# Performance work log

Hardware: AMD Instinct MI355X
Metric: run time of the kernel (lower is better)

The kernel has to match this reference:

```python
import jax, jax.numpy as jnp
import numpy as np

HIDDEN = 2048
HEADS = 16
KV_LORA = 512
ROPE_D = 64
NOPE_D = ROPE_D          # module sets qk_nope_head_dim = qk_rope_head_dim
Q_HEAD_D = ROPE_D + NOPE_D
V_D = 128
B, S = 2, 2048
SCALE = ROPE_D ** -0.5


def setup_inputs() -> dict:
    key = jax.random.key(0)
    ks = jax.random.split(key, 6)
    hidden_state = jax.random.normal(ks[0], (B, S, HIDDEN), dtype=jnp.float32)
    attention_mask = jnp.zeros((1, 1, S, S), dtype=jnp.float32)
    s = 0.02
    W_down = jax.random.normal(ks[1], (HIDDEN, KV_LORA + ROPE_D), dtype=jnp.float32) * s
    W_up = jax.random.normal(ks[2], (KV_LORA, HEADS * (NOPE_D + V_D)), dtype=jnp.float32) * s
    W_q = jax.random.normal(ks[3], (HIDDEN, HEADS * Q_HEAD_D), dtype=jnp.float32) * s
    W_o = jax.random.normal(ks[4], (HEADS * V_D, HIDDEN), dtype=jnp.float32) * s
    return {"hidden_state": hidden_state, "attention_mask": attention_mask,
            "W_down": W_down, "W_up": W_up, "W_q": W_q, "W_o": W_o}


def reference(hidden_state, attention_mask, W_down, W_up, W_q, W_o):
    b, s, _ = hidden_state.shape
    # low-rank KV down-projection; split latent and shared rope key
    kv_down = hidden_state @ W_down                      # [b,s,kv_lora+rope]
    kv_compressed = kv_down[..., :KV_LORA]
    k_rope = kv_down[..., KV_LORA:]                      # [b,s,rope]
    # up-project latent to per-head nope-key and value
    kv = (kv_compressed @ W_up).reshape(b, s, HEADS, NOPE_D + V_D)
    kv = kv.transpose(0, 2, 1, 3)                        # [b,h,s,nope+v]
    k_nope = kv[..., :NOPE_D]
    v = kv[..., NOPE_D:]
    # queries
    q = (hidden_state @ W_q).reshape(b, s, HEADS, Q_HEAD_D).transpose(0, 2, 1, 3)
    q_rope = q[..., :ROPE_D]
    q_nope = q[..., ROPE_D:]
    q_full = jnp.concatenate([q_rope, q_nope], axis=-1)  # [b,h,s,2d]
    # broadcast shared rope key across heads and concat with per-head nope key
    k_rope_exp = jnp.broadcast_to(k_rope[:, None], (b, HEADS, s, ROPE_D))
    k_full = jnp.concatenate([k_rope_exp, k_nope], axis=-1)
    scores = jnp.einsum('bhqd,bhkd->bhqk', q_full, k_full) * SCALE
    scores = scores + attention_mask
    probs = jax.nn.softmax(scores, axis=-1)
    ctx = jnp.einsum('bhqk,bhkd->bhqd', probs, v)        # [b,h,s,v]
    ctx = ctx.transpose(0, 2, 1, 3).reshape(b, s, HEADS * V_D)
    return ctx @ W_o
```

## Files before the change

kernel.cpp:

```cpp
#include <hip/hip_runtime.h>
#include <hip/hip_bf16.h>

#define HEADS   16
#define S_LEN   2048
#define BATCH   2
#define MTOT    (BATCH * S_LEN)
#define HIDDEN  2048
#define SCALE   0.125f
#define QKD_LD  2688

typedef __attribute__((ext_vector_type(8))) short          bf16x8;
typedef __attribute__((ext_vector_type(8))) unsigned short u16x8;
typedef __attribute__((ext_vector_type(4))) unsigned short u16x4;
typedef __attribute__((ext_vector_type(4))) float          f32x4;

__device__ __forceinline__ unsigned short f2bf(float f) {
    union { float f; unsigned u; } v; v.f = f;
    unsigned r = v.u + 0x7FFFu + ((v.u >> 16) & 1u);
    return (unsigned short)(r >> 16);
}

__device__ __forceinline__ unsigned cvtpk(float a, float b) {
    unsigned r;
    asm("v_cvt_pk_bf16_f32 %0, %1, %2" : "=v"(r) : "v"(a), "v"(b));
    return r;
}

__device__ __forceinline__ void gld16(const void* g, const void* l) {
    __builtin_amdgcn_global_load_lds(
        (const __attribute__((address_space(1))) void*)g,
        (__attribute__((address_space(3))) void*)l, 16, 0, 0);
}

__global__ __launch_bounds__(256)
void cast_bf16(const float* __restrict__ in, unsigned short* __restrict__ out)
{
    const size_t i = ((size_t)blockIdx.x * 256 + threadIdx.x) * 8;
    float4 a = *(const float4*)&in[i];
    float4 b = *(const float4*)&in[i + 4];
    u16x8 o;
    o[0] = f2bf(a.x); o[1] = f2bf(a.y); o[2] = f2bf(a.z); o[3] = f2bf(a.w);
    o[4] = f2bf(b.x); o[5] = f2bf(b.y); o[6] = f2bf(b.z); o[7] = f2bf(b.w);
    *(u16x8*)&out[i] = o;
}

__global__ __launch_bounds__(256)
void tc_w(const float* __restrict__ W, int N, int K, unsigned short* __restrict__ Wt)
{
    __shared__ float Tf[64][68];
    const int t  = threadIdx.x;
    const int n0 = blockIdx.x * 64, k0 = blockIdx.y * 64;
    if (n0 >= N) {
        u16x8 z = {0,0,0,0,0,0,0,0};
#pragma unroll
        for (int ii = 0; ii < 2; ii++) {
            int idx = t + 256 * ii;
            int rn = idx >> 3, c8 = (idx & 7) * 8;
            *(u16x8*)&Wt[(size_t)(n0 + rn) * K + k0 + c8] = z;
        }
        return;
    }
#pragma unroll
    for (int ii = 0; ii < 4; ii++) {
        int idx = t + 256 * ii;
        int rk = idx >> 4, c4 = (idx & 15) * 4;
        *(float4*)&Tf[rk][c4] = *(const float4*)&W[(size_t)(k0 + rk) * N + n0 + c4];
    }
    __syncthreads();
#pragma unroll
    for (int ii = 0; ii < 2; ii++) {
        int idx = t + 256 * ii;
        int rn = idx >> 3, c8 = (idx & 7) * 8;
        u16x8 o;
#pragma unroll
        for (int j = 0; j < 8; j++) o[j] = f2bf(Tf[c8 + j][rn]);
        *(u16x8*)&Wt[(size_t)(n0 + rn) * K + k0 + c8] = o;
    }
}

__global__ __launch_bounds__(256)
void transpose_v(const unsigned short* __restrict__ kvu, unsigned short* __restrict__ vT)
{
    __shared__ unsigned short Ts[64][80];
    const int t  = threadIdx.x;
    const int s0 = blockIdx.x * 64;
    const int h  = blockIdx.y >> 1, d0 = (blockIdx.y & 1) * 64;
    const int b  = blockIdx.z;
    const size_t base = (size_t)b * S_LEN;
#pragma unroll
    for (int ii = 0; ii < 2; ii++) {
        int idx = t + 256 * ii;
        int rs = idx >> 3, c8 = (idx & 7) * 8;
        *(u16x8*)&Ts[rs][c8] =
            *(const u16x8*)&kvu[(base + s0 + rs) * 3072 + h * 192 + 64 + d0 + c8];
    }
    __syncthreads();
    const size_t bh = (size_t)(b * HEADS + h);
#pragma unroll
    for (int ii = 0; ii < 2; ii++) {
        int idx = t + 256 * ii;
        int rd = idx >> 3, c8 = (idx & 7) * 8;
        u16x8 o;
#pragma unroll
        for (int j = 0; j < 8; j++) o[j] = Ts[c8 + j][rd];
        *(u16x8*)&vT[(bh * 128 + d0 + rd) * S_LEN + s0 + c8] = o;
    }
}

template<bool OUT_BF16>
__global__ __launch_bounds__(256)
void gemm_bf16(const unsigned short* __restrict__ A, int lda, int K,
               const unsigned short* __restrict__ Bt,
               void* __restrict__ C, int N, int ldc)
{
    __shared__ unsigned short As[128 * 32];
    __shared__ unsigned short Bs[128 * 32];
    const int t = threadIdx.x, lane = t & 63, w = t >> 6;
    const int l15 = lane & 15, lg = lane >> 4;
    const int row0 = blockIdx.y * 128, col0 = blockIdx.x * 128;
    const int wr = w >> 1, wc = w & 1;

    f32x4 acc[4][4] = {};

    for (int k0 = 0; k0 < K; k0 += 32) {
        __syncthreads();
#pragma unroll
        for (int ii = 0; ii < 2; ii++) {
            int u = (ii * 4 + w) * 64 + lane;
            gld16(&A[(size_t)(row0 + (u >> 2)) * lda + k0 + (u & 3) * 8],
                  (char*)As + (ii * 4 + w) * 1024);
            gld16(&Bt[(size_t)(col0 + (u >> 2)) * K + k0 + (u & 3) * 8],
                  (char*)Bs + (ii * 4 + w) * 1024);
        }
        __syncthreads();
        bf16x8 af[4], bb[4];
#pragma unroll
        for (int m = 0; m < 4; m++)
            af[m] = *(const bf16x8*)&As[(wr * 64 + m * 16 + l15) * 32 + lg * 8];
#pragma unroll
        for (int n = 0; n < 4; n++)
            bb[n] = *(const bf16x8*)&Bs[(wc * 64 + n * 16 + l15) * 32 + lg * 8];
#pragma unroll
        for (int m = 0; m < 4; m++)
#pragma unroll
            for (int n = 0; n < 4; n++)
                acc[m][n] = __builtin_amdgcn_mfma_f32_16x16x32_bf16(
                    af[m], bb[n], acc[m][n], 0, 0, 0);
    }

#pragma unroll
    for (int m = 0; m < 4; m++)
#pragma unroll
        for (int n = 0; n < 4; n++) {
            int col = col0 + wc * 64 + n * 16 + l15;
            if (col < N) {
#pragma unroll
                for (int r = 0; r < 4; r++) {
                    int row = row0 + wr * 64 + m * 16 + lg * 4 + r;
                    if (OUT_BF16)
                        ((unsigned short*)C)[(size_t)row * ldc + col] = f2bf(acc[m][n][r]);
                    else
                        ((float*)C)[(size_t)row * ldc + col] = acc[m][n][r];
                }
            }
        }
}

__global__ __launch_bounds__(256, 2)
void mla_attn_mfma(const unsigned short* __restrict__ qkd,
                   const unsigned short* __restrict__ kvu,
                   const unsigned short* __restrict__ vT,
                   const float* __restrict__ mask,
                   unsigned short* __restrict__ ctxb)
{
    __shared__ unsigned short KV[2][64 * 128 + 128 * 64];
    __shared__ unsigned short Pl[4][32 * 64];
    const int t = threadIdx.x, lane = t & 63, w = t >> 6;
    const int l15 = lane & 15, lg = lane >> 4;
    const int h = blockIdx.y, b = blockIdx.z;
    const int q0 = blockIdx.x * 128 + w * 32;
    const size_t base = (size_t)b * S_LEN;
    const size_t bh = (size_t)(b * HEADS + h);
    const unsigned short* qb = qkd + 640;
    unsigned short* Pw = &Pl[w][0];
    const unsigned psw = (unsigned)(l15 & 7) << 4;

    bf16x8 qf[2][4];
#pragma unroll
    for (int m = 0; m < 2; m++)
#pragma unroll
        for (int kk = 0; kk < 4; kk++)
            qf[m][kk] = *(const bf16x8*)&qb[(base + q0 + m * 16 + l15) * QKD_LD
                                            + h * 128 + kk * 32 + lg * 8];

    f32x4 octx[2][8] = {};
    float mrun[2] = {-INFINITY, -INFINITY};
    float lrun[2] = {0.f, 0.f};

    const float* mrow0 = &mask[(size_t)(q0 + l15) * S_LEN + lg * 4];
    const float* mrow1 = mrow0 + (size_t)16 * S_LEN;

    auto STAGE = [&](int buf, int s0) {
        unsigned short* Kb = &KV[buf][0];
        unsigned short* Vb = &KV[buf][64 * 128];
#pragma unroll
        for (int ii = 0; ii < 4; ii++) {
            int u = (ii * 4 + w) * 64 + lane;
            {
                int row = u >> 4, x = u & 15, y = x ^ (row & 7);
                const unsigned short* g = (y < 8)
                    ? &qkd[(base + s0 + row) * QKD_LD + 512 + y * 8]
                    : &kvu[(base + s0 + row) * 3072 + h * 192 + (y - 8) * 8];
                gld16(g, (char*)Kb + (ii * 4 + w) * 1024);
            }
            {
                int d = u >> 3, x = u & 7, y = x ^ (d & 7);
                gld16(&vT[(bh * 128 + d) * S_LEN + s0 + y * 8],
                      (char*)Vb + (ii * 4 + w) * 1024);
            }
        }
    };

    const int NT = S_LEN / 64;
    STAGE(0, 0);

    for (int kt = 0; kt < NT; kt++) {
        const int cur = kt & 1;
        const int s0 = kt * 64;
        const unsigned short* Ks = &KV[cur][0];
        const unsigned short* Vs = &KV[cur][64 * 128];

        __builtin_amdgcn_s_barrier();

        float4 mv[2][4];
#pragma unroll
        for (int n = 0; n < 4; n++) {
            mv[0][n] = *(const float4*)&mrow0[s0 + n * 16];
            mv[1][n] = *(const float4*)&mrow1[s0 + n * 16];
        }
        __builtin_amdgcn_sched_barrier(0);

        if (kt + 1 < NT) {
            STAGE(cur ^ 1, s0 + 64);
            __builtin_amdgcn_sched_barrier(0);
            asm volatile("s_waitcnt vmcnt(16)" ::: "memory");
        } else {
            __builtin_amdgcn_sched_barrier(0);
            asm volatile("s_waitcnt vmcnt(8)" ::: "memory");
        }
        __builtin_amdgcn_sched_barrier(0);
        __builtin_amdgcn_s_barrier();

        f32x4 sc[2][4] = {};
        __builtin_amdgcn_s_setprio(1);
#pragma unroll
        for (int n = 0; n < 4; n++) {
            const int key = n * 16 + l15;
#pragma unroll
            for (int kk = 0; kk < 4; kk++) {
                const int x = (kk * 4 + lg) ^ (key & 7);
                bf16x8 kf = *(const bf16x8*)&Ks[key * 128 + x * 8];
                sc[0][n] = __builtin_amdgcn_mfma_f32_16x16x32_bf16(kf, qf[0][kk], sc[0][n], 0, 0, 0);
                sc[1][n] = __builtin_amdgcn_mfma_f32_16x16x32_bf16(kf, qf[1][kk], sc[1][n], 0, 0, 0);
            }
        }
        __builtin_amdgcn_s_setprio(0);

        float e_bc[2][4];
#pragma unroll
        for (int m = 0; m < 2; m++) {
            float sv[4][4];
#pragma unroll
            for (int n = 0; n < 4; n++) {
                sv[n][0] = sc[m][n][0] * SCALE + mv[m][n].x;
                sv[n][1] = sc[m][n][1] * SCALE + mv[m][n].y;
                sv[n][2] = sc[m][n][2] * SCALE + mv[m][n].z;
                sv[n][3] = sc[m][n][3] * SCALE + mv[m][n].w;
            }
            float loc = sv[0][0];
#pragma unroll
            for (int n = 0; n < 4; n++)
#pragma unroll
                for (int r = 0; r < 4; r++) loc = fmaxf(loc, sv[n][r]);
            loc = fmaxf(loc, __shfl_xor(loc, 16));
            loc = fmaxf(loc, __shfl_xor(loc, 32));
            float mnew = fmaxf(mrun[m], loc);
            float esc = __expf(mrun[m] - mnew);
            mrun[m] = mnew;
            float ls = 0.f;
            const int prow = m * 16 + l15;
#pragma unroll
            for (int n = 0; n < 4; n++) {
                float p0 = __expf(sv[n][0] - mnew), p1 = __expf(sv[n][1] - mnew);
                float p2 = __expf(sv[n][2] - mnew), p3 = __expf(sv[n][3] - mnew);
                ls += (p0 + p1) + (p2 + p3);
                union { unsigned u[2]; u16x4 v; } pk;
                pk.u[0] = cvtpk(p0, p1);
                pk.u[1] = cvtpk(p2, p3);
                *(u16x4*)((char*)Pw + prow * 128 + ((n * 32 + lg * 8) ^ psw)) = pk.v;
            }
            ls += __shfl_xor(ls, 16);
            ls += __shfl_xor(ls, 32);
            lrun[m] = lrun[m] * esc + ls;
#pragma unroll
            for (int r = 0; r < 4; r++) e_bc[m][r] = __shfl(esc, lg * 4 + r);
        }

#pragma unroll
        for (int m = 0; m < 2; m++)
#pragma unroll
            for (int vn = 0; vn < 8; vn++)
#pragma unroll
                for (int r = 0; r < 4; r++) octx[m][vn][r] *= e_bc[m][r];

        asm volatile("" ::: "memory");

        bf16x8 paf[2][2];
#pragma unroll
        for (int m = 0; m < 2; m++) {
            const int prow = m * 16 + l15;
#pragma unroll
            for (int kk = 0; kk < 2; kk++)
                paf[m][kk] = *(const bf16x8*)((char*)Pw + prow * 128
                                              + ((kk * 64 + lg * 16) ^ psw));
        }
        __builtin_amdgcn_s_setprio(1);
#pragma unroll
        for (int vn = 0; vn < 8; vn++) {
            const int d = vn * 16 + l15;
#pragma unroll
            for (int kk = 0; kk < 2; kk++) {
                const int x = (kk * 4 + lg) ^ (d & 7);
                bf16x8 vf = *(const bf16x8*)&Vs[d * 64 + x * 8];
                octx[0][vn] = __builtin_amdgcn_mfma_f32_16x16x32_bf16(paf[0][kk], vf, octx[0][vn], 0, 0, 0);
                octx[1][vn] = __builtin_amdgcn_mfma_f32_16x16x32_bf16(paf[1][kk], vf, octx[1][vn], 0, 0, 0);
            }
        }
        __builtin_amdgcn_s_setprio(0);
    }

#pragma unroll
    for (int m = 0; m < 2; m++) {
        float inv[4];
#pragma unroll
        for (int r = 0; r < 4; r++) inv[r] = 1.0f / __shfl(lrun[m], lg * 4 + r);
#pragma unroll
        for (int vn = 0; vn < 8; vn++)
#pragma unroll
            for (int r = 0; r < 4; r++)
                ctxb[(base + q0 + m * 16 + lg * 4 + r) * 2048 + h * 128 + vn * 16 + l15]
                    = f2bf(octx[m][vn][r] * inv[r]);
    }
}

extern "C" void kernel_launch(void* const* d_in, const int* in_sizes, int n_in,
                              void* d_out, int out_size, void* d_ws, size_t ws_size,
                              hipStream_t stream)
{
    const float* hidden = (const float*)d_in[0];
    const float* mask   = (const float*)d_in[1];
    const float* W_down = (const float*)d_in[2];
    const float* W_up   = (const float*)d_in[3];
    const float* W_q    = (const float*)d_in[4];
    const float* W_o    = (const float*)d_in[5];
    float* out = (float*)d_out;

    unsigned short* p = (unsigned short*)d_ws;
    unsigned short* hb      = p; p += (size_t)MTOT * 2048;
    unsigned short* qkd     = p; p += (size_t)MTOT * QKD_LD;
    unsigned short* kvu_b   = p; p += (size_t)MTOT * 3072;
    unsigned short* vTb     = p; p += (size_t)BATCH * HEADS * 128 * S_LEN;
    unsigned short* ctxb    = p; p += (size_t)MTOT * 2048;
    unsigned short* Wt_cat  = p; p += (size_t)QKD_LD * 2048;
    unsigned short* Wt_up   = p; p += (size_t)3072 * 512;
    unsigned short* Wt_o    = p; p += (size_t)2048 * 2048;

    dim3 blk(256);
    cast_bf16<<<dim3(MTOT * 2048 / (256 * 8)), blk, 0, stream>>>(hidden, hb);
    tc_w<<<dim3(10, 32), blk, 0, stream>>>(W_down, 576, 2048, Wt_cat);
    tc_w<<<dim3(32, 32), blk, 0, stream>>>(W_q, 2048, 2048, Wt_cat + (size_t)640 * 2048);
    tc_w<<<dim3(48, 8),  blk, 0, stream>>>(W_up, 3072, 512, Wt_up);
    tc_w<<<dim3(32, 32), blk, 0, stream>>>(W_o, 2048, 2048, Wt_o);

    gemm_bf16<true><<<dim3(QKD_LD / 128, 32), blk, 0, stream>>>(
        hb, 2048, 2048, Wt_cat, qkd, QKD_LD, QKD_LD);
    gemm_bf16<true><<<dim3(24, 32), blk, 0, stream>>>(
        qkd, QKD_LD, 512, Wt_up, kvu_b, 3072, 3072);

    transpose_v<<<dim3(S_LEN / 64, 2 * HEADS, BATCH), blk, 0, stream>>>(kvu_b, vTb);

    mla_attn_mfma<<<dim3(S_LEN / 128, HEADS, BATCH), blk, 0, stream>>>(
        qkd, kvu_b, vTb, mask, ctxb);

    gemm_bf16<false><<<dim3(16, 32), blk, 0, stream>>>(
        ctxb, 2048, 2048, Wt_o, out, 2048, 2048);
}
```

Baseline: 297.5 us.

## Add lazy softmax rescaling with threshold and prefetch mask tiles a step ahead

Applies FA4-style conditional rescaling inside the flash-attention loop. The running max and the output accumulator are updated only when some row's new tile max exceeds the stored max by more than 8, so the per-tile exp, shuffles and 64-element scaling of the accumulator are skipped most of the time. The attention-mask tile loads are also moved one iteration ahead and issued together with the next K/V stage, with the vmcnt wait counts adjusted to match. The cost is more live registers, and probabilities can reach up to e^8 before normalization, which bf16 P values and fp32 accumulators should tolerate.

Result: no change. 297.8 us (+0.1%).

```diff
diff --git a/kernel.cpp b/kernel.cpp
--- a/kernel.cpp
+++ b/kernel.cpp
@@ -223,6 +223,12 @@
 
     const int NT = S_LEN / 64;
     STAGE(0, 0);
+    float4 mvc[2][4], mvn[2][4];
+#pragma unroll
+    for (int n = 0; n < 4; n++) {
+        mvc[0][n] = *(const float4*)&mrow0[n * 16];
+        mvc[1][n] = *(const float4*)&mrow1[n * 16];
+    }
 
     for (int kt = 0; kt < NT; kt++) {
         const int cur = kt & 1;
@@ -232,21 +238,19 @@
 
         __builtin_amdgcn_s_barrier();
 
-        float4 mv[2][4];
-#pragma unroll
-        for (int n = 0; n < 4; n++) {
-            mv[0][n] = *(const float4*)&mrow0[s0 + n * 16];
-            mv[1][n] = *(const float4*)&mrow1[s0 + n * 16];
-        }
-        __builtin_amdgcn_sched_barrier(0);
-
         if (kt + 1 < NT) {
+#pragma unroll
+            for (int n = 0; n < 4; n++) {
+                mvn[0][n] = *(const float4*)&mrow0[s0 + 64 + n * 16];
+                mvn[1][n] = *(const float4*)&mrow1[s0 + 64 + n * 16];
+            }
+            __builtin_amdgcn_sched_barrier(0);
             STAGE(cur ^ 1, s0 + 64);
             __builtin_amdgcn_sched_barrier(0);
-            asm volatile("s_waitcnt vmcnt(16)" ::: "memory");
+            asm volatile("s_waitcnt vmcnt(24)" ::: "memory");
         } else {
             __builtin_amdgcn_sched_barrier(0);
-            asm volatile("s_waitcnt vmcnt(8)" ::: "memory");
+            asm volatile("s_waitcnt vmcnt(0)" ::: "memory");
         }
         __builtin_amdgcn_sched_barrier(0);
         __builtin_amdgcn_s_barrier();
@@ -266,33 +270,52 @@
         }
         __builtin_amdgcn_s_setprio(0);
 
-        float e_bc[2][4];
+        float sv[2][4][4];
+        float loc[2];
 #pragma unroll
         for (int m = 0; m < 2; m++) {
-            float sv[4][4];
 #pragma unroll
             for (int n = 0; n < 4; n++) {
-                sv[n][0] = sc[m][n][0] * SCALE + mv[m][n].x;
-                sv[n][1] = sc[m][n][1] * SCALE + mv[m][n].y;
-                sv[n][2] = sc[m][n][2] * SCALE + mv[m][n].z;
-                sv[n][3] = sc[m][n][3] * SCALE + mv[m][n].w;
-            }
-            float loc = sv[0][0];
+                sv[m][n][0] = sc[m][n][0] * SCALE + mvc[m][n].x;
+                sv[m][n][1] = sc[m][n][1] * SCALE + mvc[m][n].y;
+                sv[m][n][2] = sc[m][n][2] * SCALE + mvc[m][n].z;
+                sv[m][n][3] = sc[m][n][3] * SCALE + mvc[m][n].w;
+            }
+            float lc = sv[m][0][0];
 #pragma unroll
             for (int n = 0; n < 4; n++)
 #pragma unroll
-                for (int r = 0; r < 4; r++) loc = fmaxf(loc, sv[n][r]);
-            loc = fmaxf(loc, __shfl_xor(loc, 16));
-            loc = fmaxf(loc, __shfl_xor(loc, 32));
-            float mnew = fmaxf(mrun[m], loc);
-            float esc = __expf(mrun[m] - mnew);
-            mrun[m] = mnew;
+                for (int r = 0; r < 4; r++) lc = fmaxf(lc, sv[m][n][r]);
+            lc = fmaxf(lc, __shfl_xor(lc, 16));
+            lc = fmaxf(lc, __shfl_xor(lc, 32));
+            loc[m] = lc;
+        }
+
+        if (!__all((int)((loc[0] <= mrun[0] + 8.f) & (loc[1] <= mrun[1] + 8.f)))) {
+#pragma unroll
+            for (int m = 0; m < 2; m++) {
+                float mnew = fmaxf(mrun[m], loc[m]);
+                float esc = __expf(mrun[m] - mnew);
+                mrun[m] = mnew;
+                lrun[m] *= esc;
+                float e_bc[4];
+#pragma unroll
+                for (int r = 0; r < 4; r++) e_bc[r] = __shfl(esc, lg * 4 + r);
+#pragma unroll
+                for (int vn = 0; vn < 8; vn++)
+#pragma unroll
+                    for (int r = 0; r < 4; r++) octx[m][vn][r] *= e_bc[r];
+            }
+        }
+
+#pragma unroll
+        for (int m = 0; m < 2; m++) {
             float ls = 0.f;
             const int prow = m * 16 + l15;
 #pragma unroll
             for (int n = 0; n < 4; n++) {
-                float p0 = __expf(sv[n][0] - mnew), p1 = __expf(sv[n][1] - mnew);
-                float p2 = __expf(sv[n][2] - mnew), p3 = __expf(sv[n][3] - mnew);
+                float p0 = __expf(sv[m][n][0] - mrun[m]), p1 = __expf(sv[m][n][1] - mrun[m]);
+                float p2 = __expf(sv[m][n][2] - mrun[m]), p3 = __expf(sv[m][n][3] - mrun[m]);
                 ls += (p0 + p1) + (p2 + p3);
                 union { unsigned u[2]; u16x4 v; } pk;
                 pk.u[0] = cvtpk(p0, p1);
@@ -301,17 +324,8 @@
             }
             ls += __shfl_xor(ls, 16);
             ls += __shfl_xor(ls, 32);
-            lrun[m] = lrun[m] * esc + ls;
-#pragma unroll
-            for (int r = 0; r < 4; r++) e_bc[m][r] = __shfl(esc, lg * 4 + r);
-        }
-
-#pragma unroll
-        for (int m = 0; m < 2; m++)
-#pragma unroll
-            for (int vn = 0; vn < 8; vn++)
-#pragma unroll
-                for (int r = 0; r < 4; r++) octx[m][vn][r] *= e_bc[m][r];
+            lrun[m] += ls;
+        }
 
         asm volatile("" ::: "memory");
 
@@ -337,6 +351,13 @@
             }
         }
         __builtin_amdgcn_s_setprio(0);
+
+        if (kt + 1 < NT) {
+#pragma unroll
+            for (int m = 0; m < 2; m++)
+#pragma unroll
+                for (int n = 0; n < 4; n++) mvc[m][n] = mvn[m][n];
+        }
     }
 
 #pragma unroll
```
